# Kernel optimization log

Hardware: AMD Instinct MI355X
Metric: run time of the kernel (lower is better)

Reference implementation:

```python
import jax, jax.numpy as jnp
import numpy as np

E = 1_000_000   # edges (temporal neighbor facts)
D = 128         # emb_dim
N = 200_000     # nodes carrying hidden state
B = 512         # queries (batch)
R = 240         # num_rel -> rel table has 2R+1 rows
T = 100_000     # tail nodes (scatter output size)


def setup_inputs() -> dict:
    key = jax.random.key(0)
    ks = jax.random.split(key, 14)
    b_col  = jax.random.randint(ks[0], (E,), 0, B)
    n_col  = jax.random.randint(ks[1], (E,), 0, N)
    h_col  = jax.random.randint(ks[2], (E,), 0, N)
    r_col  = jax.random.randint(ks[3], (E,), 0, 2 * R)   # r+1 in [1, 2R]
    t_col  = jax.random.randint(ks[4], (E,), 0, N)
    ts_col = jax.random.randint(ks[5], (E,), 0, 1000)
    facts = jnp.stack([b_col, n_col, h_col, r_col, t_col, ts_col], axis=1)
    s = 1.0 / np.sqrt(D)
    return {
        "hidden":     jax.random.normal(ks[6], (N, D), jnp.float32) * 0.02,
        "rel_table":  jax.random.normal(ks[7], (2 * R + 1, D), jnp.float32) * 0.02,
        "Ws":         jax.random.normal(ks[8], (D, D), jnp.float32) * s,
        "Wr":         jax.random.normal(ks[9], (D, D), jnp.float32) * s,
        "Wqr_w":      jax.random.normal(ks[10], (D, D), jnp.float32) * s,
        "Wqr_b":      jnp.zeros((D,), jnp.float32),
        "wa_w":       jax.random.normal(ks[11], (D, 1), jnp.float32) * s,
        "wa_b":       jnp.zeros((1,), jnp.float32),
        "Wh":         jax.random.normal(ks[12], (D, D), jnp.float32) * s,
        "query_rel":  jax.random.randint(ks[13], (B,), 0, 2 * R),
        "facts":      facts,
        "tail_index": jax.random.randint(jax.random.fold_in(key, 99), (E,), 0, T),
        "tail_nodes": jnp.arange(T),
    }


def reference(hidden, rel_table, Ws, Wr, Wqr_w, Wqr_b, wa_w, wa_b, Wh,
              query_rel, facts, tail_index, tail_nodes):
    b = facts[:, 0]
    n = facts[:, 1]
    r = facts[:, 3]
    h_e = hidden[n]                      # [E, D] gather node hidden
    hr  = rel_table[r + 1]               # [E, D] gather relation emb
    q_r = rel_table[query_rel + 1][b]    # [E, D] per-edge query relation
    # attention MLP: sigmoid(w_alpha(relu(Ws h + Wr r + Wqr q + b)))
    pre = h_e @ Ws + hr @ Wr + (q_r @ Wqr_w + Wqr_b)          # [E, D]
    alpha = jax.nn.sigmoid(jax.nn.relu(pre) @ wa_w + wa_b)    # [E, 1]
    message = alpha * (h_e + hr)                              # [E, D]
    agg = jax.ops.segment_sum(message, tail_index,
                              num_segments=tail_nodes.shape[0])  # [T, D]
    return agg @ Wh                      # act = identity (default)
```

## Files before the change

kernel.cpp:

```cpp
#include <hip/hip_runtime.h>
#include <hip/hip_fp16.h>
#include <math.h>

#define DD 128
#define CAP 64

typedef _Float16 half_t;
typedef __attribute__((ext_vector_type(8))) _Float16 half8;
typedef __attribute__((ext_vector_type(4))) float floatx4;

#define LDW 136

__device__ __forceinline__ __half2 relu2(__half2 x) {
    return __hmul2(x, __hgt2(x, __float2half2_rn(0.f)));
}

template <int CTRL>
__device__ __forceinline__ float dpp_add(float x) {
    int y = __builtin_amdgcn_update_dpp(0, __float_as_int(x), CTRL, 0xf, 0xf, true);
    return x + __int_as_float(y);
}

__global__ void wt4(const float* __restrict__ W0, const float* __restrict__ W1,
                    const float* __restrict__ W2, const float* __restrict__ W3,
                    half_t* __restrict__ T0, half_t* __restrict__ T1,
                    half_t* __restrict__ T2, half_t* __restrict__ T3) {
    const float* W = blockIdx.x == 0 ? W0 : blockIdx.x == 1 ? W1 : blockIdx.x == 2 ? W2 : W3;
    half_t* T      = blockIdx.x == 0 ? T0 : blockIdx.x == 1 ? T1 : blockIdx.x == 2 ? T2 : T3;
    for (int i = threadIdx.x; i < DD * DD; i += blockDim.x) {
        int n = i >> 7, k = i & 127;
        T[i] = (half_t)W[(size_t)k * DD + n];
    }
}

__global__ __launch_bounds__(256) void gemm_mfma(
    const float* __restrict__ table, const int* __restrict__ idx, int idxAdd, int M,
    const half_t* __restrict__ WT_g, const float* __restrict__ bias,
    float* __restrict__ OutF, __half* __restrict__ OutH) {
    __shared__ half_t WT[DD * LDW];
    __shared__ half_t As[64 * LDW];
    int tid = threadIdx.x;
    int lane = tid & 63;
    int w = tid >> 6;
    int rowf = lane & 15;
    int kgrp = (lane >> 4) * 8;

    for (int i = tid; i < 2048; i += 256) {
        int n = i >> 4, ch = i & 15;
        *(half8*)(WT + n * LDW + ch * 8) = *(const half8*)(WT_g + n * DD + ch * 8);
    }
    int tileM = blockIdx.x * 64;
    for (int i = tid; i < 2048; i += 256) {
        int row = i >> 5, c4 = i & 31;
        int gr = tileM + row;
        float4 v = make_float4(0.f, 0.f, 0.f, 0.f);
        if (gr < M) {
            int src = idx ? (idx[gr] + idxAdd) : gr;
            v = *(const float4*)(table + (size_t)src * DD + c4 * 4);
        }
        __half2 h01 = __floats2half2_rn(v.x, v.y);
        __half2 h23 = __floats2half2_rn(v.z, v.w);
        *(uint2*)(As + row * LDW + c4 * 4) = make_uint2(*(unsigned*)&h01, *(unsigned*)&h23);
    }
    __syncthreads();

    floatx4 acc[8];
#pragma unroll
    for (int t = 0; t < 8; t++) acc[t] = (floatx4){0.f, 0.f, 0.f, 0.f};
    const half_t* ap = As + (w * 16 + rowf) * LDW + kgrp;
    const half_t* bp0 = WT + rowf * LDW + kgrp;
#pragma unroll
    for (int kk = 0; kk < DD; kk += 32) {
        half8 a = *(const half8*)(ap + kk);
#pragma unroll
        for (int t = 0; t < 8; t++) {
            half8 b = *(const half8*)(bp0 + t * 16 * LDW + kk);
            acc[t] = __builtin_amdgcn_mfma_f32_16x16x32_f16(a, b, acc[t], 0, 0, 0);
        }
    }
    int orow = tileM + w * 16 + (lane >> 4) * 4;
#pragma unroll
    for (int t = 0; t < 8; t++) {
        int col = t * 16 + rowf;
        float bv = bias ? bias[col] : 0.f;
#pragma unroll
        for (int i = 0; i < 4; i++) {
            int gr = orow + i;
            if (gr < M) {
                float o = acc[t][i] + bv;
                if (OutF) OutF[(size_t)gr * DD + col] = o;
                if (OutH) OutH[(size_t)gr * DD + col] = __float2half(o);
            }
        }
    }
}

__global__ __launch_bounds__(256) void gemm_pack_mfma(
    const float* __restrict__ table, int M,
    const half_t* __restrict__ WT_g, __half* __restrict__ Packed) {
    __shared__ half_t WT[DD * LDW];
    __shared__ half_t As[64 * LDW];
    int tid = threadIdx.x;
    int lane = tid & 63;
    int w = tid >> 6;
    int rowf = lane & 15;
    int kgrp = (lane >> 4) * 8;

    for (int i = tid; i < 2048; i += 256) {
        int n = i >> 4, ch = i & 15;
        *(half8*)(WT + n * LDW + ch * 8) = *(const half8*)(WT_g + n * DD + ch * 8);
    }
    int tileM = blockIdx.x * 64;
    for (int i = tid; i < 2048; i += 256) {
        int row = i >> 5, c4 = i & 31;
        int gr = tileM + row;
        float4 v = make_float4(0.f, 0.f, 0.f, 0.f);
        if (gr < M) v = *(const float4*)(table + (size_t)gr * DD + c4 * 4);
        __half2 h01 = __floats2half2_rn(v.x, v.y);
        __half2 h23 = __floats2half2_rn(v.z, v.w);
        uint2 u = make_uint2(*(unsigned*)&h01, *(unsigned*)&h23);
        *(uint2*)(As + row * LDW + c4 * 4) = u;
        if (gr < M) *(uint2*)(Packed + (size_t)gr * 256 + c4 * 4) = u;
    }
    __syncthreads();

    floatx4 acc[8];
#pragma unroll
    for (int t = 0; t < 8; t++) acc[t] = (floatx4){0.f, 0.f, 0.f, 0.f};
    const half_t* ap = As + (w * 16 + rowf) * LDW + kgrp;
    const half_t* bp0 = WT + rowf * LDW + kgrp;
#pragma unroll
    for (int kk = 0; kk < DD; kk += 32) {
        half8 a = *(const half8*)(ap + kk);
#pragma unroll
        for (int t = 0; t < 8; t++) {
            half8 b = *(const half8*)(bp0 + t * 16 * LDW + kk);
            acc[t] = __builtin_amdgcn_mfma_f32_16x16x32_f16(a, b, acc[t], 0, 0, 0);
        }
    }
    int orow = tileM + w * 16 + (lane >> 4) * 4;
#pragma unroll
    for (int t = 0; t < 8; t++) {
        int col = t * 16 + rowf;
#pragma unroll
        for (int i = 0; i < 4; i++) {
            int gr = orow + i;
            if (gr < M) Packed[(size_t)gr * 256 + 128 + col] = __float2half(acc[t][i]);
        }
    }
}

__global__ __launch_bounds__(256) void alpha_scatter(
    const __half* __restrict__ HB, const __half* __restrict__ RB,
    const __half* __restrict__ QB, const int* __restrict__ facts,
    const int* __restrict__ tail, const float* __restrict__ wa,
    const float* __restrict__ wa_b,
    int* __restrict__ cursor, int2* __restrict__ meta, int E) {
    int tid = threadIdx.x;
    int lane = tid & 63;
    int g = lane >> 4;
    int cl = lane & 15;
    int c = cl * 8;
    int wv = (blockIdx.x * 256 + tid) >> 6;
    int e0 = wv * 8 + g;

    float4 wva = *(const float4*)(wa + c);
    float4 wvb = *(const float4*)(wa + c + 4);
    __half2 w0 = __halves2half2(__float2half(wva.x), __float2half(wva.y));
    __half2 w1 = __halves2half2(__float2half(wva.z), __float2half(wva.w));
    __half2 w2 = __halves2half2(__float2half(wvb.x), __float2half(wvb.y));
    __half2 w3 = __halves2half2(__float2half(wvb.z), __float2half(wvb.w));
    float wb = wa_b[0];

    int f0 = e0, f1 = e0 + 4;
    bool v0 = f0 < E, v1 = f1 < E;
    int fc0 = v0 ? f0 : 0, fc1 = v1 ? f1 : 0;

    int2 bn0 = *(const int2*)(facts + (size_t)fc0 * 6);
    int r0 = facts[(size_t)fc0 * 6 + 3];
    int tl0 = tail[fc0];
    int2 bn1 = *(const int2*)(facts + (size_t)fc1 * 6);
    int r1 = facts[(size_t)fc1 * 6 + 3];
    int tl1 = tail[fc1];

    uint4 h0 = *(const uint4*)(HB + (size_t)bn0.y * 256 + 128 + c);
    uint4 rr0 = *(const uint4*)(RB + (size_t)(r0 + 1) * 256 + 128 + c);
    uint4 q0 = *(const uint4*)(QB + (size_t)bn0.x * DD + c);
    uint4 h1 = *(const uint4*)(HB + (size_t)bn1.y * 256 + 128 + c);
    uint4 rr1 = *(const uint4*)(RB + (size_t)(r1 + 1) * 256 + 128 + c);
    uint4 q1 = *(const uint4*)(QB + (size_t)bn1.x * DD + c);

#define DOT8(hu, ru, qu, out)                                                          \
    {                                                                                  \
        __half2 p0 = relu2(__hadd2(__hadd2(*(__half2*)&(hu).x, *(__half2*)&(ru).x),    \
                                   *(__half2*)&(qu).x));                               \
        __half2 p1 = relu2(__hadd2(__hadd2(*(__half2*)&(hu).y, *(__half2*)&(ru).y),    \
                                   *(__half2*)&(qu).y));                               \
        __half2 p2 = relu2(__hadd2(__hadd2(*(__half2*)&(hu).z, *(__half2*)&(ru).z),    \
                                   *(__half2*)&(qu).z));                               \
        __half2 p3 = relu2(__hadd2(__hadd2(*(__half2*)&(hu).w, *(__half2*)&(ru).w),    \
                                   *(__half2*)&(qu).w));                               \
        __half2 t2 = __hfma2(p1, w1, __hmul2(p0, w0));                                 \
        t2 = __hfma2(p2, w2, t2);                                                      \
        t2 = __hfma2(p3, w3, t2);                                                      \
        out = __half2float(__low2half(t2)) + __half2float(__high2half(t2));            \
    }
    float t0, t1;
    DOT8(h0, rr0, q0, t0);
    DOT8(h1, rr1, q1, t1);
#undef DOT8

    t0 = dpp_add<0x111>(t0); t0 = dpp_add<0x112>(t0);
    t0 = dpp_add<0x114>(t0); t0 = dpp_add<0x118>(t0);
    t1 = dpp_add<0x111>(t1); t1 = dpp_add<0x112>(t1);
    t1 = dpp_add<0x114>(t1); t1 = dpp_add<0x118>(t1);

    if (cl == 15) {
        float a0 = 1.f / (1.f + __expf(-(t0 + wb)));
        float a1 = 1.f / (1.f + __expf(-(t1 + wb)));
        unsigned ab0 = (unsigned)__half_as_ushort(__float2half(a0));
        unsigned ab1 = (unsigned)__half_as_ushort(__float2half(a1));
        if (v0) {
            int slot = atomicAdd(&cursor[tl0], 1);
            if (slot < CAP)
                meta[(size_t)tl0 * CAP + slot] = make_int2(bn0.y, (r0 + 1) | (int)(ab0 << 16));
        }
        if (v1) {
            int slot = atomicAdd(&cursor[tl1], 1);
            if (slot < CAP)
                meta[(size_t)tl1 * CAP + slot] = make_int2(bn1.y, (r1 + 1) | (int)(ab1 << 16));
        }
    }
}

__global__ __launch_bounds__(256) void agg_lite(
    const __half* __restrict__ HB, const __half* __restrict__ RB,
    const int2* __restrict__ meta, const int* __restrict__ cursor,
    float* __restrict__ agg, int T) {
    int w = threadIdx.x >> 6;
    int lane = threadIdx.x & 63;
    int seg = blockIdx.x * 4 + w;
    if (seg >= T) return;
    int cnt = cursor[seg];
    if (cnt > CAP) cnt = CAP;
    const int2* mp = meta + (size_t)seg * CAP;
    int co = lane * 2;
    float ax = 0.f, ay = 0.f;

#define ACC(hu, ru, y_)                                                        \
    {                                                                          \
        __half2 s = __hadd2(*(__half2*)&(hu), *(__half2*)&(ru));               \
        float al =                                                             \
            __half2float(__ushort_as_half((unsigned short)((unsigned)(y_) >> 16))); \
        float2 sf = __half22float2(s);                                         \
        ax = fmaf(al, sf.x, ax);                                               \
        ay = fmaf(al, sf.y, ay);                                               \
    }

    int i = 0;
    for (; i + 3 < cnt; i += 4) {
        int4 ma = *(const int4*)(mp + i);
        int4 mb = *(const int4*)(mp + i + 2);
        unsigned h0 = *(const unsigned*)(HB + (size_t)ma.x * 256 + co);
        unsigned r0 = *(const unsigned*)(RB + (size_t)(ma.y & 0xFFFF) * 256 + co);
        unsigned h1 = *(const unsigned*)(HB + (size_t)ma.z * 256 + co);
        unsigned r1 = *(const unsigned*)(RB + (size_t)(ma.w & 0xFFFF) * 256 + co);
        unsigned h2 = *(const unsigned*)(HB + (size_t)mb.x * 256 + co);
        unsigned r2 = *(const unsigned*)(RB + (size_t)(mb.y & 0xFFFF) * 256 + co);
        unsigned h3 = *(const unsigned*)(HB + (size_t)mb.z * 256 + co);
        unsigned r3 = *(const unsigned*)(RB + (size_t)(mb.w & 0xFFFF) * 256 + co);
        ACC(h0, r0, ma.y);
        ACC(h1, r1, ma.w);
        ACC(h2, r2, mb.y);
        ACC(h3, r3, mb.w);
    }
    for (; i < cnt; i++) {
        int2 m = mp[i];
        unsigned hu = *(const unsigned*)(HB + (size_t)m.x * 256 + co);
        unsigned ru = *(const unsigned*)(RB + (size_t)(m.y & 0xFFFF) * 256 + co);
        ACC(hu, ru, m.y);
    }
#undef ACC

    *(float2*)(agg + (size_t)seg * DD + co) = make_float2(ax, ay);
}

extern "C" void kernel_launch(void* const* d_in, const int* in_sizes, int n_in,
                              void* d_out, int out_size, void* d_ws, size_t ws_size,
                              hipStream_t stream) {
    const float* hidden    = (const float*)d_in[0];
    const float* rel_table = (const float*)d_in[1];
    const float* Ws        = (const float*)d_in[2];
    const float* Wr        = (const float*)d_in[3];
    const float* Wqr_w     = (const float*)d_in[4];
    const float* Wqr_b     = (const float*)d_in[5];
    const float* wa_w      = (const float*)d_in[6];
    const float* wa_b      = (const float*)d_in[7];
    const float* Wh        = (const float*)d_in[8];
    const int* query_rel   = (const int*)d_in[9];
    const int* facts       = (const int*)d_in[10];
    const int* tail_index  = (const int*)d_in[11];

    int N     = in_sizes[0] / DD;
    int Rrows = in_sizes[1] / DD;
    int B     = in_sizes[9];
    int E     = in_sizes[11];
    int T     = in_sizes[12];

    char* ws = (char*)d_ws;
    size_t off = 0;
    auto alloc = [&](size_t bytes) -> void* {
        void* p = ws + off;
        off += (bytes + 255) & ~(size_t)255;
        return p;
    };
    __half* HB  = (__half*)alloc((size_t)N * 256 * 2);
    __half* RB  = (__half*)alloc((size_t)Rrows * 256 * 2);
    __half* QB  = (__half*)alloc((size_t)B * DD * 2);
    int* cursor = (int*)alloc((size_t)T * 4);
    int2* meta  = (int2*)alloc((size_t)T * CAP * 8);
    float* agg  = (float*)alloc((size_t)T * DD * 4);
    half_t* WsT  = (half_t*)alloc((size_t)DD * DD * 2);
    half_t* WrT  = (half_t*)alloc((size_t)DD * DD * 2);
    half_t* WqrT = (half_t*)alloc((size_t)DD * DD * 2);
    half_t* WhT  = (half_t*)alloc((size_t)DD * DD * 2);

    (void)hipMemsetAsync(cursor, 0, (size_t)T * 4, stream);

    wt4<<<4, 256, 0, stream>>>(Ws, Wr, Wqr_w, Wh, WsT, WrT, WqrT, WhT);

    gemm_pack_mfma<<<(N + 63) / 64, 256, 0, stream>>>(hidden, N, WsT, HB);
    gemm_pack_mfma<<<(Rrows + 63) / 64, 256, 0, stream>>>(rel_table, Rrows, WrT, RB);
    gemm_mfma<<<(B + 63) / 64, 256, 0, stream>>>(rel_table, query_rel, 1, B,
                                                 WqrT, Wqr_b, nullptr, QB);

    alpha_scatter<<<(E + 31) / 32, 256, 0, stream>>>(HB, RB, QB, facts, tail_index,
                                                     wa_w, wa_b, cursor, meta, E);

    agg_lite<<<(T + 3) / 4, 256, 0, stream>>>(HB, RB, meta, cursor, agg, T);

    gemm_mfma<<<(T + 63) / 64, 256, 0, stream>>>(agg, nullptr, 0, T, WhT, nullptr,
                                                 (float*)d_out, nullptr);
}
```

Baseline: 472.3 us.

## Fold output projection Wh into node and relation tables before aggregation

Uses linearity of the segment sum to apply Wh to the hidden and relation tables up front. The packed first half of each table now holds h@Wh and r@Wh instead of the raw fp16 rows, so the aggregation kernel writes the final output directly. This removes the final T-row GEMM and the fp32 agg round trip through memory. In exchange, each pack block runs a second MFMA pass over N rows and reloads the weight tile into shared memory. The aggregation loop is also unrolled to eight edges per iteration to keep more gathers in flight.

```diff
diff --git a/kernel.cpp b/kernel.cpp
--- a/kernel.cpp
+++ b/kernel.cpp
@@ -31,6 +31,72 @@
         int n = i >> 7, k = i & 127;
         T[i] = (half_t)W[(size_t)k * DD + n];
     }
+}
+
+__device__ __forceinline__ void mfma_pass_store(
+    const half_t* As, const half_t* WT, int tileM, int M, int w, int lane,
+    __half* Packed, int halfOff) {
+    int rowf = lane & 15;
+    int kgrp = (lane >> 4) * 8;
+    floatx4 acc[8];
+#pragma unroll
+    for (int t = 0; t < 8; t++) acc[t] = (floatx4){0.f, 0.f, 0.f, 0.f};
+    const half_t* ap = As + (w * 16 + rowf) * LDW + kgrp;
+    const half_t* bp0 = WT + rowf * LDW + kgrp;
+#pragma unroll
+    for (int kk = 0; kk < DD; kk += 32) {
+        half8 a = *(const half8*)(ap + kk);
+#pragma unroll
+        for (int t = 0; t < 8; t++) {
+            half8 b = *(const half8*)(bp0 + t * 16 * LDW + kk);
+            acc[t] = __builtin_amdgcn_mfma_f32_16x16x32_f16(a, b, acc[t], 0, 0, 0);
+        }
+    }
+    int orow = tileM + w * 16 + (lane >> 4) * 4;
+#pragma unroll
+    for (int t = 0; t < 8; t++) {
+        int col = t * 16 + rowf;
+#pragma unroll
+        for (int i = 0; i < 4; i++) {
+            int gr = orow + i;
+            if (gr < M) Packed[(size_t)gr * 256 + halfOff + col] = __float2half(acc[t][i]);
+        }
+    }
+}
+
+__global__ __launch_bounds__(256) void gemm_pack2(
+    const float* __restrict__ table, int M,
+    const half_t* __restrict__ WT1_g, const half_t* __restrict__ WT2_g,
+    __half* __restrict__ Packed) {
+    __shared__ half_t WT[DD * LDW];
+    __shared__ half_t As[64 * LDW];
+    int tid = threadIdx.x;
+    int lane = tid & 63;
+    int w = tid >> 6;
+    int tileM = blockIdx.x * 64;
+
+    for (int i = tid; i < 2048; i += 256) {
+        int row = i >> 5, c4 = i & 31;
+        int gr = tileM + row;
+        float4 v = make_float4(0.f, 0.f, 0.f, 0.f);
+        if (gr < M) v = *(const float4*)(table + (size_t)gr * DD + c4 * 4);
+        __half2 h01 = __floats2half2_rn(v.x, v.y);
+        __half2 h23 = __floats2half2_rn(v.z, v.w);
+        *(uint2*)(As + row * LDW + c4 * 4) = make_uint2(*(unsigned*)&h01, *(unsigned*)&h23);
+    }
+    for (int i = tid; i < 2048; i += 256) {
+        int n = i >> 4, ch = i & 15;
+        *(half8*)(WT + n * LDW + ch * 8) = *(const half8*)(WT1_g + n * DD + ch * 8);
+    }
+    __syncthreads();
+    mfma_pass_store(As, WT, tileM, M, w, lane, Packed, 0);
+    __syncthreads();
+    for (int i = tid; i < 2048; i += 256) {
+        int n = i >> 4, ch = i & 15;
+        *(half8*)(WT + n * LDW + ch * 8) = *(const half8*)(WT2_g + n * DD + ch * 8);
+    }
+    __syncthreads();
+    mfma_pass_store(As, WT, tileM, M, w, lane, Packed, 128);
 }
 
 __global__ __launch_bounds__(256) void gemm_mfma(
@@ -91,61 +157,6 @@
                 if (OutF) OutF[(size_t)gr * DD + col] = o;
                 if (OutH) OutH[(size_t)gr * DD + col] = __float2half(o);
             }
-        }
-    }
-}
-
-__global__ __launch_bounds__(256) void gemm_pack_mfma(
-    const float* __restrict__ table, int M,
-    const half_t* __restrict__ WT_g, __half* __restrict__ Packed) {
-    __shared__ half_t WT[DD * LDW];
-    __shared__ half_t As[64 * LDW];
-    int tid = threadIdx.x;
-    int lane = tid & 63;
-    int w = tid >> 6;
-    int rowf = lane & 15;
-    int kgrp = (lane >> 4) * 8;
-
-    for (int i = tid; i < 2048; i += 256) {
-        int n = i >> 4, ch = i & 15;
-        *(half8*)(WT + n * LDW + ch * 8) = *(const half8*)(WT_g + n * DD + ch * 8);
-    }
-    int tileM = blockIdx.x * 64;
-    for (int i = tid; i < 2048; i += 256) {
-        int row = i >> 5, c4 = i & 31;
-        int gr = tileM + row;
-        float4 v = make_float4(0.f, 0.f, 0.f, 0.f);
-        if (gr < M) v = *(const float4*)(table + (size_t)gr * DD + c4 * 4);
-        __half2 h01 = __floats2half2_rn(v.x, v.y);
-        __half2 h23 = __floats2half2_rn(v.z, v.w);
-        uint2 u = make_uint2(*(unsigned*)&h01, *(unsigned*)&h23);
-        *(uint2*)(As + row * LDW + c4 * 4) = u;
-        if (gr < M) *(uint2*)(Packed + (size_t)gr * 256 + c4 * 4) = u;
-    }
-    __syncthreads();
-
-    floatx4 acc[8];
-#pragma unroll
-    for (int t = 0; t < 8; t++) acc[t] = (floatx4){0.f, 0.f, 0.f, 0.f};
-    const half_t* ap = As + (w * 16 + rowf) * LDW + kgrp;
-    const half_t* bp0 = WT + rowf * LDW + kgrp;
-#pragma unroll
-    for (int kk = 0; kk < DD; kk += 32) {
-        half8 a = *(const half8*)(ap + kk);
-#pragma unroll
-        for (int t = 0; t < 8; t++) {
-            half8 b = *(const half8*)(bp0 + t * 16 * LDW + kk);
-            acc[t] = __builtin_amdgcn_mfma_f32_16x16x32_f16(a, b, acc[t], 0, 0, 0);
-        }
-    }
-    int orow = tileM + w * 16 + (lane >> 4) * 4;
-#pragma unroll
-    for (int t = 0; t < 8; t++) {
-        int col = t * 16 + rowf;
-#pragma unroll
-        for (int i = 0; i < 4; i++) {
-            int gr = orow + i;
-            if (gr < M) Packed[(size_t)gr * 256 + 128 + col] = __float2half(acc[t][i]);
         }
     }
 }
@@ -233,10 +244,10 @@
     }
 }
 
-__global__ __launch_bounds__(256) void agg_lite(
+__global__ __launch_bounds__(256) void agg_out(
     const __half* __restrict__ HB, const __half* __restrict__ RB,
     const int2* __restrict__ meta, const int* __restrict__ cursor,
-    float* __restrict__ agg, int T) {
+    float* __restrict__ out, int T) {
     int w = threadIdx.x >> 6;
     int lane = threadIdx.x & 63;
     int seg = blockIdx.x * 4 + w;
@@ -258,6 +269,32 @@
     }
 
     int i = 0;
+    for (; i + 7 < cnt; i += 8) {
+        int4 ma = *(const int4*)(mp + i);
+        int4 mb = *(const int4*)(mp + i + 2);
+        int4 mc = *(const int4*)(mp + i + 4);
+        int4 md = *(const int4*)(mp + i + 6);
+        unsigned h0 = *(const unsigned*)(HB + (size_t)ma.x * 256 + co);
+        unsigned r0 = *(const unsigned*)(RB + (size_t)(ma.y & 0xFFFF) * 256 + co);
+        unsigned h1 = *(const unsigned*)(HB + (size_t)ma.z * 256 + co);
+        unsigned r1 = *(const unsigned*)(RB + (size_t)(ma.w & 0xFFFF) * 256 + co);
+        unsigned h2 = *(const unsigned*)(HB + (size_t)mb.x * 256 + co);
+        unsigned r2 = *(const unsigned*)(RB + (size_t)(mb.y & 0xFFFF) * 256 + co);
+        unsigned h3 = *(const unsigned*)(HB + (size_t)mb.z * 256 + co);
+        unsigned r3 = *(const unsigned*)(RB + (size_t)(mb.w & 0xFFFF) * 256 + co);
+        unsigned h4 = *(const unsigned*)(HB + (size_t)mc.x * 256 + co);
+        unsigned r4 = *(const unsigned*)(RB + (size_t)(mc.y & 0xFFFF) * 256 + co);
+        unsigned h5 = *(const unsigned*)(HB + (size_t)mc.z * 256 + co);
+        unsigned r5 = *(const unsigned*)(RB + (size_t)(mc.w & 0xFFFF) * 256 + co);
+        unsigned h6 = *(const unsigned*)(HB + (size_t)md.x * 256 + co);
+        unsigned r6 = *(const unsigned*)(RB + (size_t)(md.y & 0xFFFF) * 256 + co);
+        unsigned h7 = *(const unsigned*)(HB + (size_t)md.z * 256 + co);
+        unsigned r7 = *(const unsigned*)(RB + (size_t)(md.w & 0xFFFF) * 256 + co);
+        ACC(h0, r0, ma.y); ACC(h1, r1, ma.w);
+        ACC(h2, r2, mb.y); ACC(h3, r3, mb.w);
+        ACC(h4, r4, mc.y); ACC(h5, r5, mc.w);
+        ACC(h6, r6, md.y); ACC(h7, r7, md.w);
+    }
     for (; i + 3 < cnt; i += 4) {
         int4 ma = *(const int4*)(mp + i);
         int4 mb = *(const int4*)(mp + i + 2);
@@ -269,10 +306,8 @@
         unsigned r2 = *(const unsigned*)(RB + (size_t)(mb.y & 0xFFFF) * 256 + co);
         unsigned h3 = *(const unsigned*)(HB + (size_t)mb.z * 256 + co);
         unsigned r3 = *(const unsigned*)(RB + (size_t)(mb.w & 0xFFFF) * 256 + co);
-        ACC(h0, r0, ma.y);
-        ACC(h1, r1, ma.w);
-        ACC(h2, r2, mb.y);
-        ACC(h3, r3, mb.w);
+        ACC(h0, r0, ma.y); ACC(h1, r1, ma.w);
+        ACC(h2, r2, mb.y); ACC(h3, r3, mb.w);
     }
     for (; i < cnt; i++) {
         int2 m = mp[i];
@@ -282,7 +317,7 @@
     }
 #undef ACC
 
-    *(float2*)(agg + (size_t)seg * DD + co) = make_float2(ax, ay);
+    *(float2*)(out + (size_t)seg * DD + co) = make_float2(ax, ay);
 }
 
 extern "C" void kernel_launch(void* const* d_in, const int* in_sizes, int n_in,
@@ -319,7 +354,6 @@
     __half* QB  = (__half*)alloc((size_t)B * DD * 2);
     int* cursor = (int*)alloc((size_t)T * 4);
     int2* meta  = (int2*)alloc((size_t)T * CAP * 8);
-    float* agg  = (float*)alloc((size_t)T * DD * 4);
     half_t* WsT  = (half_t*)alloc((size_t)DD * DD * 2);
     half_t* WrT  = (half_t*)alloc((size_t)DD * DD * 2);
     half_t* WqrT = (half_t*)alloc((size_t)DD * DD * 2);
@@ -329,16 +363,14 @@
 
     wt4<<<4, 256, 0, stream>>>(Ws, Wr, Wqr_w, Wh, WsT, WrT, WqrT, WhT);
 
-    gemm_pack_mfma<<<(N + 63) / 64, 256, 0, stream>>>(hidden, N, WsT, HB);
-    gemm_pack_mfma<<<(Rrows + 63) / 64, 256, 0, stream>>>(rel_table, Rrows, WrT, RB);
+    gemm_pack2<<<(N + 63) / 64, 256, 0, stream>>>(hidden, N, WhT, WsT, HB);
+    gemm_pack2<<<(Rrows + 63) / 64, 256, 0, stream>>>(rel_table, Rrows, WhT, WrT, RB);
     gemm_mfma<<<(B + 63) / 64, 256, 0, stream>>>(rel_table, query_rel, 1, B,
                                                  WqrT, Wqr_b, nullptr, QB);
 
     alpha_scatter<<<(E + 31) / 32, 256, 0, stream>>>(HB, RB, QB, facts, tail_index,
                                                      wa_w, wa_b, cursor, meta, E);
 
-    agg_lite<<<(T + 3) / 4, 256, 0, stream>>>(HB, RB, meta, cursor, agg, T);
-
-    gemm_mfma<<<(T + 63) / 64, 256, 0, stream>>>(agg, nullptr, 0, T, WhT, nullptr,
-                                                 (float*)d_out, nullptr);
-}
+    agg_out<<<(T + 3) / 4, 256, 0, stream>>>(HB, RB, meta, cursor,
+                                             (float*)d_out, T);
+}
```

Result: faster. 451.7 us (-4.4%).
